# Optimization experiments

Measured on AMD Instinct MI355X. Metric: run time of the kernel, lower is better.

The kernel has to match this reference:

```python
import jax, jax.numpy as jnp
import numpy as np

N_HEAD = 16
ROPE_BASE = 10000.0


def _rotate_every_two(x):
    # x: [..., d]; pairs (x0,x1) -> (-x1, x0) interleaved (GPT-J style)
    x1 = x[..., ::2]
    x2 = x[..., 1::2]
    return jnp.stack((-x2, x1), axis=-1).reshape(x.shape)


def _rope_cos_sin(T, head_dim, dtype):
    inv_freq = 1.0 / (ROPE_BASE ** (jnp.arange(0, head_dim, 2, dtype=jnp.float32) / head_dim))
    t = jnp.arange(T, dtype=jnp.float32)
    freqs = t[:, None] * inv_freq[None, :]            # [T, hd/2]
    emb = jnp.repeat(freqs, 2, axis=-1)               # [T, hd], each freq duplicated
    return jnp.cos(emb).astype(dtype)[None, None], jnp.sin(emb).astype(dtype)[None, None]


def setup_inputs() -> dict:
    key = jax.random.key(0)
    k1, k2, k3 = jax.random.split(key, 3)
    C = 2048
    x = jax.random.normal(k1, (2, 2048, C), dtype=jnp.float32)
    Wqkv = jax.random.normal(k2, (C, 3 * C), dtype=jnp.float32) * 0.02   # c_attn.weight^T
    Wproj = jax.random.normal(k3, (C, C), dtype=jnp.float32) * 0.02      # c_proj.weight^T
    return {"x": x, "Wqkv": Wqkv, "Wproj": Wproj, "causal": 1}


def reference(x, Wqkv, Wproj, causal):
    B, T, C = x.shape
    H = N_HEAD
    hd = C // H

    qkv = x @ Wqkv                                    # [B,T,3C]
    q, k, v = jnp.split(qkv, 3, axis=-1)
    # -> [B,H,T,hd]
    q = q.reshape(B, T, H, hd).transpose(0, 2, 1, 3)
    k = k.reshape(B, T, H, hd).transpose(0, 2, 1, 3)
    v = v.reshape(B, T, H, hd).transpose(0, 2, 1, 3)

    cos, sin = _rope_cos_sin(T, hd, x.dtype)          # [1,1,T,hd]
    q = q * cos + _rotate_every_two(q) * sin
    k = k * cos + _rotate_every_two(k) * sin

    scale = 1.0 / jnp.sqrt(jnp.asarray(hd, dtype=x.dtype))
    scores = jnp.einsum('bhqd,bhkd->bhqk', q, k) * scale  # [B,H,T,T]
    if causal:
        mask = jnp.tril(jnp.ones((T, T), dtype=bool))
        scores = jnp.where(mask[None, None], scores, jnp.asarray(-1e30, dtype=scores.dtype))
    attn = jax.nn.softmax(scores, axis=-1)
    y = jnp.einsum('bhqk,bhkd->bhqd', attn, v)        # [B,H,T,hd]
    y = y.transpose(0, 2, 1, 3).reshape(B, T, C)
    return y @ Wproj
```

## Files before the change

kernel.cpp:

```cpp
#include <hip/hip_runtime.h>
#include <cmath>

typedef __bf16 bf16_t;
typedef __bf16 bf16x8 __attribute__((ext_vector_type(8)));
typedef __bf16 bf16x4 __attribute__((ext_vector_type(4)));
typedef float f32x4 __attribute__((ext_vector_type(4)));

#define T_SEQ 2048
#define C_DIM 2048
#define H_NUM 16
#define HD    128
#define KK    2048

__global__ void rope_table_kernel(float* __restrict__ ct, float* __restrict__ st) {
  int idx = blockIdx.x * 256 + threadIdx.x;
  int t = idx >> 6, i = idx & 63;
  double invf = pow(10000.0, -(double)i / 64.0);
  float ang = (float)t * (float)invf;
  ct[idx] = cosf(ang);
  st[idx] = sinf(ang);
}

__global__ void convert_bf16_kernel(const float* __restrict__ in, bf16_t* __restrict__ out, int n4) {
  int i = blockIdx.x * 256 + threadIdx.x;
  if (i >= n4) return;
  const float4 v = reinterpret_cast<const float4*>(in)[i];
  bf16x4 o;
  o[0] = (bf16_t)v.x; o[1] = (bf16_t)v.y; o[2] = (bf16_t)v.z; o[3] = (bf16_t)v.w;
  reinterpret_cast<bf16x4*>(out)[i] = o;
}

__global__ void transpose_convert_kernel(const float* __restrict__ in, bf16_t* __restrict__ out,
                                         int R, int Cc) {
  __shared__ __align__(16) bf16_t tile[32][33];
  int c0 = blockIdx.x * 32, r0 = blockIdx.y * 32;
  int tx = threadIdx.x, ty = threadIdx.y;
#pragma unroll
  for (int i = 0; i < 4; ++i)
    tile[ty + 8 * i][tx] = (bf16_t)in[(size_t)(r0 + ty + 8 * i) * Cc + c0 + tx];
  __syncthreads();
#pragma unroll
  for (int i = 0; i < 4; ++i)
    out[(size_t)(c0 + ty + 8 * i) * R + r0 + tx] = tile[tx][ty + 8 * i];
}

template <int MODE>
__global__ __launch_bounds__(256, 2)
void gemm_bf16_kernel(const bf16_t* __restrict__ A, const bf16_t* __restrict__ Bt,
                      float* __restrict__ outF,
                      bf16_t* __restrict__ qws, bf16_t* __restrict__ kws,
                      bf16_t* __restrict__ vtws,
                      const float* __restrict__ ctab, const float* __restrict__ stab) {
  const int tid = threadIdx.x;
  const int l = tid & 63, w = tid >> 6;
  const int wr = w >> 1, wc = w & 1;
  const int m0 = blockIdx.y * 128, n0 = blockIdx.x * 128;
  const int lg = l >> 4, lr = l & 15;

  __shared__ __align__(16) bf16_t la[128][72];
  __shared__ __align__(16) bf16_t lb[128][72];

  f32x4 acc[4][4] = {};
  bf16x8 ra[4], rb[4];

  const bf16_t* Ab = A + (size_t)m0 * KK;
  const bf16_t* Bb = Bt + (size_t)n0 * KK;

#pragma unroll
  for (int c = 0; c < 4; ++c) {
    int p = tid + c * 256, row = p >> 3, kc = p & 7;
    ra[c] = *reinterpret_cast<const bf16x8*>(Ab + (size_t)row * KK + kc * 8);
    rb[c] = *reinterpret_cast<const bf16x8*>(Bb + (size_t)row * KK + kc * 8);
  }

  for (int kt = 0; kt < KK / 64; ++kt) {
    __syncthreads();
#pragma unroll
    for (int c = 0; c < 4; ++c) {
      int p = tid + c * 256, row = p >> 3, kc = p & 7;
      *reinterpret_cast<bf16x8*>(&la[row][kc * 8]) = ra[c];
      *reinterpret_cast<bf16x8*>(&lb[row][kc * 8]) = rb[c];
    }
    __syncthreads();
    if (kt + 1 < KK / 64) {
#pragma unroll
      for (int c = 0; c < 4; ++c) {
        int p = tid + c * 256, row = p >> 3, kc = p & 7;
        ra[c] = *reinterpret_cast<const bf16x8*>(Ab + (size_t)row * KK + (kt + 1) * 64 + kc * 8);
        rb[c] = *reinterpret_cast<const bf16x8*>(Bb + (size_t)row * KK + (kt + 1) * 64 + kc * 8);
      }
    }
#pragma unroll
    for (int ks = 0; ks < 2; ++ks) {
      bf16x8 af[4], bfr[4];
#pragma unroll
      for (int i = 0; i < 4; ++i) {
        af[i]  = *reinterpret_cast<const bf16x8*>(&la[wr * 64 + i * 16 + lr][ks * 32 + lg * 8]);
        bfr[i] = *reinterpret_cast<const bf16x8*>(&lb[wc * 64 + i * 16 + lr][ks * 32 + lg * 8]);
      }
#pragma unroll
      for (int mi = 0; mi < 4; ++mi)
#pragma unroll
        for (int ni = 0; ni < 4; ++ni)
          acc[mi][ni] = __builtin_amdgcn_mfma_f32_16x16x32_bf16(af[mi], bfr[ni], acc[mi][ni], 0, 0, 0);
    }
  }

  if (MODE == 0) {
    const int sec = n0 >> 11;
    const int h = (n0 & 2047) >> 7;
#pragma unroll
    for (int mi = 0; mi < 4; ++mi) {
#pragma unroll
      for (int ni = 0; ni < 4; ++ni) {
        const int d = wc * 64 + ni * 16 + lr;
#pragma unroll
        for (int r = 0; r < 4; ++r) {
          const int m = m0 + wr * 64 + mi * 16 + lg * 4 + r;
          const int b = m >> 11, t = m & 2047;
          float val = acc[mi][ni][r];
          if (sec < 2) {
            float partner = __shfl_xor(val, 1);
            const int fi = d >> 1;
            float cth = ctab[t * 64 + fi], sth = stab[t * 64 + fi];
            float ov = (d & 1) ? (val * cth + partner * sth)
                               : (val * cth - partner * sth);
            if (sec == 0) ov *= 0.08838834764831845f;
            bf16_t* dst = (sec == 0) ? qws : kws;
            dst[((size_t)(b * H_NUM + h) * T_SEQ + t) * HD + d] = (bf16_t)ov;
          } else {
            vtws[((size_t)(b * H_NUM + h) * HD + d) * T_SEQ + t] = (bf16_t)val;
          }
        }
      }
    }
  } else {
#pragma unroll
    for (int mi = 0; mi < 4; ++mi)
#pragma unroll
      for (int ni = 0; ni < 4; ++ni) {
        const int n = n0 + wc * 64 + ni * 16 + lr;
#pragma unroll
        for (int r = 0; r < 4; ++r) {
          const int m = m0 + wr * 64 + mi * 16 + lg * 4 + r;
          outF[(size_t)m * C_DIM + n] = acc[mi][ni][r];
        }
      }
  }
}

__global__ __launch_bounds__(256, 2)
void attention_kernel(const bf16_t* __restrict__ qg, const bf16_t* __restrict__ kg,
                      const bf16_t* __restrict__ vtg, bf16_t* __restrict__ yg) {
  const int tid = threadIdx.x;
  const int l = tid & 63, w = tid >> 6;
  const int lg = l >> 4, lr = l & 15;
  const int bh = blockIdx.y;
  const int b = bh >> 4, h = bh & 15;

  __shared__ __align__(16) bf16_t lk[2][64][128];
  __shared__ __align__(16) bf16_t lp[4][16][72];

  const bf16_t* qp = qg + (size_t)bh * T_SEQ * HD;
  const bf16_t* kp = kg + (size_t)bh * T_SEQ * HD;
  const bf16_t* vp = vtg + (size_t)bh * HD * T_SEQ;

#pragma unroll 1
  for (int half = 0; half < 2; ++half) {
    const int qt = (half == 0) ? (31 - blockIdx.x) : blockIdx.x;
    const int qbase = qt * 64 + w * 16;

    bf16x8 qf[4];
#pragma unroll
    for (int dk = 0; dk < 4; ++dk)
      qf[dk] = *reinterpret_cast<const bf16x8*>(qp + (size_t)(qbase + lr) * HD + dk * 32 + lg * 8);

    f32x4 o[8] = {};
    float mrun[4], lrun[4];
#pragma unroll
    for (int r = 0; r < 4; ++r) { mrun[r] = -1e30f; lrun[r] = 0.f; }

    bf16x8 kreg[4];
#pragma unroll
    for (int c = 0; c < 4; ++c) {
      int p = tid + c * 256, row = p >> 4, ch = p & 15;
      kreg[c] = *reinterpret_cast<const bf16x8*>(kp + (size_t)row * HD + ch * 8);
    }
    __syncthreads();
#pragma unroll
    for (int c = 0; c < 4; ++c) {
      int p = tid + c * 256, row = p >> 4, ch = (p & 15) ^ (row & 7);
      *reinterpret_cast<bf16x8*>(&lk[0][row][ch * 8]) = kreg[c];
    }
    __syncthreads();

#pragma unroll 1
    for (int kt = 0; kt <= qt; ++kt) {
      const int cur = kt & 1;
      const int kv0 = kt * 64;

      bf16x8 vf[16];
#pragma unroll
      for (int cc = 0; cc < 8; ++cc)
#pragma unroll
        for (int ks = 0; ks < 2; ++ks)
          vf[cc * 2 + ks] = *reinterpret_cast<const bf16x8*>(
              vp + (size_t)(cc * 16 + lr) * T_SEQ + kv0 + ks * 32 + lg * 8);

      if (kt < qt) {
#pragma unroll
        for (int c = 0; c < 4; ++c) {
          int p = tid + c * 256, row = p >> 4, ch = p & 15;
          kreg[c] = *reinterpret_cast<const bf16x8*>(
              kp + (size_t)(kv0 + 64 + row) * HD + ch * 8);
        }
      }

      f32x4 sacc[4] = {};
#pragma unroll
      for (int dk = 0; dk < 4; ++dk) {
        bf16x8 kf[4];
#pragma unroll
        for (int f = 0; f < 4; ++f) {
          const int ch = (dk * 4 + lg) ^ (lr & 7);
          kf[f] = *reinterpret_cast<const bf16x8*>(&lk[cur][f * 16 + lr][ch * 8]);
        }
#pragma unroll
        for (int f = 0; f < 4; ++f)
          sacc[f] = __builtin_amdgcn_mfma_f32_16x16x32_bf16(qf[dk], kf[f], sacc[f], 0, 0, 0);
      }

      if (kt == qt) {
#pragma unroll
        for (int f = 0; f < 4; ++f)
#pragma unroll
          for (int r = 0; r < 4; ++r)
            if (kv0 + f * 16 + lr > qbase + lg * 4 + r) sacc[f][r] = -1e30f;
      }

      float sf[4];
#pragma unroll
      for (int r = 0; r < 4; ++r) {
        float mx = fmaxf(fmaxf(sacc[0][r], sacc[1][r]), fmaxf(sacc[2][r], sacc[3][r]));
        mx = fmaxf(mx, __shfl_xor(mx, 1));
        mx = fmaxf(mx, __shfl_xor(mx, 2));
        mx = fmaxf(mx, __shfl_xor(mx, 4));
        mx = fmaxf(mx, __shfl_xor(mx, 8));
        float mnew = fmaxf(mrun[r], mx);
        sf[r] = __expf(mrun[r] - mnew);
        mrun[r] = mnew;
      }
#pragma unroll
      for (int f = 0; f < 4; ++f)
#pragma unroll
        for (int r = 0; r < 4; ++r)
          sacc[f][r] = __expf(sacc[f][r] - mrun[r]);
#pragma unroll
      for (int r = 0; r < 4; ++r) {
        float s = sacc[0][r] + sacc[1][r] + sacc[2][r] + sacc[3][r];
        s += __shfl_xor(s, 1); s += __shfl_xor(s, 2);
        s += __shfl_xor(s, 4); s += __shfl_xor(s, 8);
        lrun[r] = lrun[r] * sf[r] + s;
      }
#pragma unroll
      for (int cc = 0; cc < 8; ++cc)
#pragma unroll
        for (int r = 0; r < 4; ++r)
          o[cc][r] *= sf[r];

#pragma unroll
      for (int f = 0; f < 4; ++f)
#pragma unroll
        for (int r = 0; r < 4; ++r)
          lp[w][lg * 4 + r][f * 16 + lr] = (bf16_t)sacc[f][r];

#pragma unroll
      for (int ks = 0; ks < 2; ++ks) {
        bf16x8 pf = *reinterpret_cast<const bf16x8*>(&lp[w][lr][ks * 32 + lg * 8]);
#pragma unroll
        for (int cc = 0; cc < 8; ++cc)
          o[cc] = __builtin_amdgcn_mfma_f32_16x16x32_bf16(pf, vf[cc * 2 + ks], o[cc], 0, 0, 0);
      }

      if (kt < qt) {
#pragma unroll
        for (int c = 0; c < 4; ++c) {
          int p = tid + c * 256, row = p >> 4, ch = (p & 15) ^ (row & 7);
          *reinterpret_cast<bf16x8*>(&lk[cur ^ 1][row][ch * 8]) = kreg[c];
        }
      }
      __syncthreads();
    }

#pragma unroll
    for (int r = 0; r < 4; ++r) lrun[r] = 1.0f / lrun[r];
#pragma unroll
    for (int cc = 0; cc < 8; ++cc)
#pragma unroll
      for (int r = 0; r < 4; ++r) {
        int t = qbase + lg * 4 + r;
        float val = o[cc][r] * lrun[r];
        yg[((size_t)(b * T_SEQ + t)) * C_DIM + h * HD + cc * 16 + lr] = (bf16_t)val;
      }
  }
}

extern "C" void kernel_launch(void* const* d_in, const int* in_sizes, int n_in,
                              void* d_out, int out_size, void* d_ws, size_t ws_size,
                              hipStream_t stream) {
  (void)in_sizes; (void)n_in; (void)out_size; (void)ws_size;
  const float* x     = (const float*)d_in[0];
  const float* Wqkv  = (const float*)d_in[1];
  const float* Wproj = (const float*)d_in[2];
  float* out = (float*)d_out;

  char* ws = (char*)d_ws;
  float*  ctab   = (float*)(ws + 0);
  float*  stab   = (float*)(ws + 524288);
  bf16_t* xb     = (bf16_t*)(ws + 1048576);
  bf16_t* wqkvT  = (bf16_t*)(ws + 17825792);
  bf16_t* wprojT = (bf16_t*)(ws + 42991616);
  bf16_t* qws    = (bf16_t*)(ws + 51380224);
  bf16_t* kws    = (bf16_t*)(ws + 68157440);
  bf16_t* vtws   = (bf16_t*)(ws + 84934656);
  bf16_t* yws    = (bf16_t*)(ws + 101711872);

  rope_table_kernel<<<512, 256, 0, stream>>>(ctab, stab);
  convert_bf16_kernel<<<8192, 256, 0, stream>>>(x, xb, 2097152);
  transpose_convert_kernel<<<dim3(192, 64), dim3(32, 8), 0, stream>>>(Wqkv, wqkvT, 2048, 6144);
  transpose_convert_kernel<<<dim3(64, 64), dim3(32, 8), 0, stream>>>(Wproj, wprojT, 2048, 2048);

  gemm_bf16_kernel<0><<<dim3(48, 32), 256, 0, stream>>>(
      xb, wqkvT, nullptr, qws, kws, vtws, ctab, stab);

  attention_kernel<<<dim3(16, 32), 256, 0, stream>>>(qws, kws, vtws, yws);

  gemm_bf16_kernel<1><<<dim3(16, 32), 256, 0, stream>>>(
      yws, wprojT, out, nullptr, nullptr, nullptr, nullptr, nullptr);
}
```

Baseline: 363.9 us.

## Swizzle GEMM LDS tiles, fold log2e into Q scale, add lazy softmax rescale

The GEMM shared-memory tiles drop their padding and use an XOR swizzle of 16-byte chunks, which keeps LDS reads conflict-free in less space. The Q scale now includes log2(e), so attention can use exp2f in place of __expf. Attention also skips rescaling the running max, sum and output accumulator unless some row's max grows by more than 8 in log2 units, checked wave-wide. This cuts exp and multiply work in the softmax loop, at the cost of exp values up to 2^8 feeding the bf16 P matrix and the fp32 accumulators.

Result: no change. 359.5 us (-1.2%).

```diff
diff --git a/kernel.cpp b/kernel.cpp
--- a/kernel.cpp
+++ b/kernel.cpp
@@ -57,8 +57,8 @@
   const int m0 = blockIdx.y * 128, n0 = blockIdx.x * 128;
   const int lg = l >> 4, lr = l & 15;
 
-  __shared__ __align__(16) bf16_t la[128][72];
-  __shared__ __align__(16) bf16_t lb[128][72];
+  __shared__ __align__(16) bf16_t la[128][64];
+  __shared__ __align__(16) bf16_t lb[128][64];
 
   f32x4 acc[4][4] = {};
   bf16x8 ra[4], rb[4];
@@ -77,9 +77,10 @@
     __syncthreads();
 #pragma unroll
     for (int c = 0; c < 4; ++c) {
-      int p = tid + c * 256, row = p >> 3, kc = p & 7;
-      *reinterpret_cast<bf16x8*>(&la[row][kc * 8]) = ra[c];
-      *reinterpret_cast<bf16x8*>(&lb[row][kc * 8]) = rb[c];
+      int p = tid + c * 256, row = p >> 3;
+      int kcw = (p & 7) ^ (row & 7);
+      *reinterpret_cast<bf16x8*>(&la[row][kcw * 8]) = ra[c];
+      *reinterpret_cast<bf16x8*>(&lb[row][kcw * 8]) = rb[c];
     }
     __syncthreads();
     if (kt + 1 < KK / 64) {
@@ -93,10 +94,11 @@
 #pragma unroll
     for (int ks = 0; ks < 2; ++ks) {
       bf16x8 af[4], bfr[4];
+      const int pc = ((ks * 4 + lg) ^ (lr & 7)) * 8;
 #pragma unroll
       for (int i = 0; i < 4; ++i) {
-        af[i]  = *reinterpret_cast<const bf16x8*>(&la[wr * 64 + i * 16 + lr][ks * 32 + lg * 8]);
-        bfr[i] = *reinterpret_cast<const bf16x8*>(&lb[wc * 64 + i * 16 + lr][ks * 32 + lg * 8]);
+        af[i]  = *reinterpret_cast<const bf16x8*>(&la[wr * 64 + i * 16 + lr][pc]);
+        bfr[i] = *reinterpret_cast<const bf16x8*>(&lb[wc * 64 + i * 16 + lr][pc]);
       }
 #pragma unroll
       for (int mi = 0; mi < 4; ++mi)
@@ -125,7 +127,7 @@
             float cth = ctab[t * 64 + fi], sth = stab[t * 64 + fi];
             float ov = (d & 1) ? (val * cth + partner * sth)
                                : (val * cth - partner * sth);
-            if (sec == 0) ov *= 0.08838834764831845f;
+            if (sec == 0) ov *= 0.127517445f;
             bf16_t* dst = (sec == 0) ? qws : kws;
             dst[((size_t)(b * H_NUM + h) * T_SEQ + t) * HD + d] = (bf16_t)ov;
           } else {
@@ -238,35 +240,41 @@
             if (kv0 + f * 16 + lr > qbase + lg * 4 + r) sacc[f][r] = -1e30f;
       }
 
-      float sf[4];
+      float mx[4];
 #pragma unroll
       for (int r = 0; r < 4; ++r) {
-        float mx = fmaxf(fmaxf(sacc[0][r], sacc[1][r]), fmaxf(sacc[2][r], sacc[3][r]));
-        mx = fmaxf(mx, __shfl_xor(mx, 1));
-        mx = fmaxf(mx, __shfl_xor(mx, 2));
-        mx = fmaxf(mx, __shfl_xor(mx, 4));
-        mx = fmaxf(mx, __shfl_xor(mx, 8));
-        float mnew = fmaxf(mrun[r], mx);
-        sf[r] = __expf(mrun[r] - mnew);
-        mrun[r] = mnew;
+        float m = fmaxf(fmaxf(sacc[0][r], sacc[1][r]), fmaxf(sacc[2][r], sacc[3][r]));
+        m = fmaxf(m, __shfl_xor(m, 1));
+        m = fmaxf(m, __shfl_xor(m, 2));
+        m = fmaxf(m, __shfl_xor(m, 4));
+        m = fmaxf(m, __shfl_xor(m, 8));
+        mx[r] = m;
+      }
+      bool grow = (mx[0] > mrun[0] + 8.f) || (mx[1] > mrun[1] + 8.f) ||
+                  (mx[2] > mrun[2] + 8.f) || (mx[3] > mrun[3] + 8.f);
+      if (__any(grow)) {
+#pragma unroll
+        for (int r = 0; r < 4; ++r) {
+          float mnew = fmaxf(mrun[r], mx[r]);
+          float sf = exp2f(mrun[r] - mnew);
+          mrun[r] = mnew;
+          lrun[r] *= sf;
+#pragma unroll
+          for (int cc = 0; cc < 8; ++cc) o[cc][r] *= sf;
+        }
       }
 #pragma unroll
       for (int f = 0; f < 4; ++f)
 #pragma unroll
         for (int r = 0; r < 4; ++r)
-          sacc[f][r] = __expf(sacc[f][r] - mrun[r]);
+          sacc[f][r] = exp2f(sacc[f][r] - mrun[r]);
 #pragma unroll
       for (int r = 0; r < 4; ++r) {
         float s = sacc[0][r] + sacc[1][r] + sacc[2][r] + sacc[3][r];
         s += __shfl_xor(s, 1); s += __shfl_xor(s, 2);
         s += __shfl_xor(s, 4); s += __shfl_xor(s, 8);
-        lrun[r] = lrun[r] * sf[r] + s;
-      }
-#pragma unroll
-      for (int cc = 0; cc < 8; ++cc)
-#pragma unroll
-        for (int r = 0; r < 4; ++r)
-          o[cc][r] *= sf[r];
+        lrun[r] += s;
+      }
 
 #pragma unroll
       for (int f = 0; f < 4; ++f)
```
